# Kernel tuning notes

Hardware: AMD Instinct MI355X
Metric: run time of the kernel (lower is better)

Reference implementation:

```python
import jax, jax.numpy as jnp
import numpy as np

EPS = 1e-8
NU_MOLECULAR = 1.5e-05
# loss weights (module defaults)
DATA_W, BC_W, TURB_W, RANS_W, SMOOTH_W, WALL_W = 1.0, 0.05, 0.05, 0.05, 0.01, 0.02
CONT_INIT = CONT_TGT = 0.1
MOM_INIT = MOM_TGT = 0.1
RAMP_STEPS, RAMP_START = 1000, 0

N_NODES, N_EDGES = 100000, 6400000


def _curriculum_weights(step):
    if step < RAMP_START:
        return CONT_INIT, MOM_INIT
    if step >= RAMP_START + RAMP_STEPS:
        return CONT_TGT, MOM_TGT
    alpha = (step - RAMP_START) / RAMP_STEPS  # linear ramp
    return ((1 - alpha) * CONT_INIT + alpha * CONT_TGT,
            (1 - alpha) * MOM_INIT + alpha * MOM_TGT)


def setup_inputs() -> dict:
    key = jax.random.key(0)
    k1, k2, k3, k4, k5 = jax.random.split(key, 5)
    predictions = jax.random.normal(k1, (N_NODES, 4), dtype=jnp.float32)
    targets = jax.random.normal(k2, (N_NODES, 4), dtype=jnp.float32)
    # dx, dy strictly positive edge offsets
    edge_attr_dxdy = jax.random.uniform(k3, (N_EDGES, 2), dtype=jnp.float32, minval=1e-3, maxval=0.05)
    edge_index = jax.random.randint(k4, (2, N_EDGES), 0, N_NODES, dtype=jnp.int64)
    wall_mask = jax.random.bernoulli(k5, 0.05, (N_NODES,))
    return {"predictions": predictions, "targets": targets,
            "edge_attr_dxdy": edge_attr_dxdy, "edge_index": edge_index,
            "wall_mask": wall_mask, "step": 500}


def reference(predictions, targets, edge_attr_dxdy, edge_index, wall_mask, step):
    cont_w, mom_w = _curriculum_weights(int(step))
    N = predictions.shape[0]
    row, col = edge_index[0], edge_index[1]
    u, v, p, nu_t = (predictions[:, i] for i in range(4))
    dx, dy = edge_attr_dxdy[:, 0], edge_attr_dxdy[:, 1]

    # per-edge finite differences (single gather of node fields)
    du = u[col] - u[row]
    dv = v[col] - v[row]
    dp = p[col] - p[row]

    seg = lambda e: jax.ops.segment_sum(e, row, num_segments=N)
    edge_count = jnp.maximum(seg(jnp.ones_like(du)), 1.0)

    # --- data loss ---
    mse_loss = jnp.mean((predictions - targets) ** 2)

    # --- continuity (divergence) loss ---
    divergence = (seg(du / (dx + EPS)) + seg(dv / (dy + EPS))) / edge_count
    div_loss = jnp.mean(divergence ** 2)

    # --- momentum loss ---
    p_grad_x = seg(dp / (dx + EPS)) / edge_count
    p_grad_y = seg(dp / (dy + EPS)) / edge_count
    lap_u = seg(du / (dx ** 2 + EPS)) / edge_count
    lap_v = seg(dv / (dy ** 2 + EPS)) / edge_count
    nu_eff = NU_MOLECULAR + nu_t
    momentum_loss = jnp.mean((p_grad_x + nu_eff * lap_u) ** 2 +
                             (p_grad_y + nu_eff * lap_v) ** 2)

    # --- turbulence losses ---
    positivity_loss = jnp.mean(jax.nn.relu(-nu_t) ** 2)
    du_dx = du / (dx + EPS)
    du_dy = du / (dy + EPS)
    dv_dx = dv / (dx + EPS)
    dv_dy = dv / (dy + EPS)
    strain_sq_edge = 2.0 * (du_dx ** 2 + dv_dy ** 2) + (du_dy + dv_dx) ** 2
    strain_node = seg(strain_sq_edge) / edge_count
    production = nu_t * strain_node
    turb_production_loss = jnp.mean(production ** 2)
    turb_dissipation_loss = jnp.mean(nu_t ** 2)

    # --- boundary-condition & wall-function losses (wall mask) ---
    m = wall_mask.astype(u.dtype)
    n_wall = jnp.maximum(jnp.sum(m), 1.0)
    bc_loss = jnp.sum(m * (u ** 2 + v ** 2)) / n_wall
    wall_loss = jnp.sum(m * (u ** 2 + v ** 2 + nu_t ** 2)) / n_wall

    # --- smoothness loss over edges ---
    smooth_loss = jnp.mean((predictions[col] - predictions[row]) ** 2)

    total = (DATA_W * mse_loss + cont_w * div_loss + mom_w * momentum_loss +
             TURB_W * turb_production_loss + RANS_W * turb_dissipation_loss +
             BC_W * bc_loss + SMOOTH_W * smooth_loss + WALL_W * wall_loss)
    # positivity_loss is tracked but not weighted into total (per visible code paths)
    return total
```

## Files before the change

kernel.cpp:

```cpp
#include <hip/hip_runtime.h>
#include <hip/hip_fp16.h>

#define EPS 1e-8f
#define NU_MOL 1.5e-5f
#define NPB 512
#define MAXNB 256
#define NBP 256
#define NBLK 4096
#define CMAX 1664
#define KMAX 7
#define CH 2048
#define SPLIT 6
#define NGRP 64
#define GRP 64


union U32H2 { unsigned u; __half2 h; };

__device__ inline unsigned packh2(float a, float b) {
    U32H2 x; x.h = __halves2half2(__float2half_rn(a), __float2half_rn(b));
    return x.u;
}
__device__ inline float2 unpackh2(unsigned u) {
    U32H2 x; x.u = u;
    return make_float2(__low2float(x.h), __high2float(x.h));
}
__device__ inline unsigned bf16rne(float f) {
    unsigned u = __float_as_uint(f);
    u += 0x7FFFu + ((u >> 16) & 1u);
    return u >> 16;
}
__device__ inline float bf16dec(unsigned h) {
    return __uint_as_float(h << 16);
}


__global__ void detect_idx_dtype(const void* eidx, int N, int* flag) {
    const long long* ll = (const long long*)eidx;
    int is64 = 1;
    for (int i = 0; i < 16; ++i) {
        long long v = ll[i];
        if (v < 0 || v >= (long long)N) { is64 = 0; break; }
    }
    *flag = is64;
}

__global__ void finalize_kernel(const double* __restrict__ d,
                                const double* __restrict__ smooth_slots,
                                int N, int E, float* __restrict__ out)
{
    double smooth = 0.0;
    for (int i = 0; i < 64; ++i) smooth += smooth_slots[i];
    double dN = (double)N;
    double n_wall = d[5] > 1.0 ? d[5] : 1.0;
    double total = 1.0  * d[0] / (4.0 * dN)
                 + 0.1  * d[1] / dN
                 + 0.1  * d[2] / dN
                 + 0.05 * d[3] / dN
                 + 0.05 * d[4] / dN
                 + 0.05 * d[6] / n_wall
                 + 0.01 * smooth / (4.0 * (double)E)
                 + 0.02 * d[7] / n_wall;
    out[0] = (float)total;
}


__global__ __launch_bounds__(256) void count_kernel(
    const void* __restrict__ eidx, int E, int N, int NB,
    const int* __restrict__ flag, unsigned* __restrict__ counts)
{
    __shared__ unsigned hist[2][MAXNB];
    hist[0][threadIdx.x] = 0u;
    hist[1][threadIdx.x] = 0u;
    __syncthreads();
    const int w = (threadIdx.x >> 6) & 1;
    const int is64 = *flag;
    const long long* ll = (const long long*)eidx;
    const int* ii = (const int*)eidx;
    int chunk = (E + NBLK - 1) / NBLK;
    int s = blockIdx.x * chunk;
    int eend = min(E, s + chunk);
    for (int e = s + (int)threadIdx.x; e < eend; e += 256) {
        int r = is64 ? (int)ll[e] : ii[e];
        r = min(max(r, 0), N - 1);
        atomicAdd(&hist[w][r >> 9], 1u);
    }
    __syncthreads();
    if (threadIdx.x < NB)
        counts[(size_t)blockIdx.x * NBP + threadIdx.x] =
            hist[0][threadIdx.x] + hist[1][threadIdx.x];
}

__global__ __launch_bounds__(256) void group_sums_kernel(
    const unsigned* __restrict__ counts, unsigned* __restrict__ gsum, int NB)
{
    __shared__ unsigned red[4][64];
    int g = blockIdx.x;
    int b0 = blockIdx.y * 64;
    int j = threadIdx.x & 63, seg = threadIdx.x >> 6;
    int b = b0 + j;
    unsigned ssum = 0;
    if (b < NB) {
        #pragma unroll
        for (int k = 0; k < 16; ++k) {
            int row = g * GRP + seg * 16 + k;
            ssum += counts[(size_t)row * NBP + b];
        }
    }
    red[seg][j] = ssum;
    __syncthreads();
    if (seg == 0 && b < NB)
        gsum[(size_t)g * NBP + b] = red[0][j] + red[1][j] + red[2][j] + red[3][j];
}

__global__ __launch_bounds__(512) void scan_base_kernel(
    unsigned* __restrict__ gsum, unsigned* __restrict__ base, int NB)
{
    __shared__ unsigned sc[512];
    int t = threadIdx.x;
    unsigned total = 0;
    if (t < NB)
        for (int g = 0; g < NGRP; ++g) total += gsum[(size_t)g * NBP + t];
    sc[t] = total; __syncthreads();
    for (int off = 1; off < 512; off <<= 1) {
        unsigned x = (t >= off) ? sc[t - off] : 0u;
        __syncthreads();
        sc[t] += x;
        __syncthreads();
    }
    unsigned ex = sc[t] - total;
    if (t < NB) {
        base[t] = ex;
        unsigned run = ex;
        for (int g = 0; g < NGRP; ++g) {
            unsigned x = gsum[(size_t)g * NBP + t];
            gsum[(size_t)g * NBP + t] = run;
            run += x;
        }
    }
    if (t == 511) base[NB] = sc[511];
}

__global__ __launch_bounds__(256) void local_scan_kernel(
    unsigned* __restrict__ counts, const unsigned* __restrict__ gsum, int NB)
{
    __shared__ unsigned segs[4][64];
    int g = blockIdx.x;
    int b0 = blockIdx.y * 64;
    int j = threadIdx.x & 63, seg = threadIdx.x >> 6;
    int b = b0 + j;
    unsigned v[16];
    unsigned ssum = 0;
    if (b < NB) {
        #pragma unroll
        for (int k = 0; k < 16; ++k) {
            int row = g * GRP + seg * 16 + k;
            v[k] = counts[(size_t)row * NBP + b];
            ssum += v[k];
        }
    }
    segs[seg][j] = ssum;
    __syncthreads();
    if (b < NB) {
        unsigned carry = gsum[(size_t)g * NBP + b];
        for (int s_ = 0; s_ < seg; ++s_) carry += segs[s_][j];
        #pragma unroll
        for (int k = 0; k < 16; ++k) {
            int row = g * GRP + seg * 16 + k;
            counts[(size_t)row * NBP + b] = carry;
            carry += v[k];
        }
    }
}

__global__ __launch_bounds__(256) void scatter_kernel(
    const void* __restrict__ eidx, const float2* __restrict__ eattr,
    int E, int N, int NB, const int* __restrict__ flag,
    const unsigned* __restrict__ localoff ,
    uint2* __restrict__ vals)
{
    __shared__ unsigned hist[2][MAXNB];
    __shared__ unsigned cur[MAXNB];
    __shared__ unsigned gb2[MAXNB];
    __shared__ uint2 pl[CMAX];
    __shared__ unsigned char bb[CMAX];
    __shared__ unsigned wt[4];

    const int t = threadIdx.x;
    const int blk = blockIdx.x;
    const int lane = t & 63, wv = t >> 6;
    const int w = wv & 1;
    const int is64 = *flag;
    const long long* ll = (const long long*)eidx;
    const int* ii = (const int*)eidx;
    const int chunk = (E + NBLK - 1) / NBLK;
    const int s = blk * chunk;
    const int Cb = min(chunk, E - s);

    hist[0][t] = 0u;
    hist[1][t] = 0u;
    __syncthreads();

    unsigned rr[KMAX];
    #pragma unroll
    for (int k = 0; k < KMAX; ++k) {
        int i = k * 256 + t;
        if (i < Cb) {
            int r = is64 ? (int)ll[s + i] : ii[s + i];
            r = min(max(r, 0), N - 1);
            rr[k] = (unsigned)r;
            atomicAdd(&hist[w][r >> 9], 1u);
        } else rr[k] = 0xFFFFFFFFu;
    }
    if (t < NB) gb2[t] = localoff[(size_t)blk * NBP + t];
    __syncthreads();

    unsigned h = hist[0][t] + hist[1][t];
    unsigned x = h;
    #pragma unroll
    for (int off = 1; off < 64; off <<= 1) {
        unsigned y = (unsigned)__shfl_up((int)x, off, 64);
        if (lane >= off) x += y;
    }
    if (lane == 63) wt[wv] = x;
    __syncthreads();
    unsigned wadd = 0;
    for (int w2 = 0; w2 < wv; ++w2) wadd += wt[w2];
    unsigned ex = x + wadd - h;
    hist[0][t] = ex;
    cur[t] = ex;
    __syncthreads();
    if (t < NB) gb2[t] -= hist[0][t];
    __syncthreads();

    #pragma unroll
    for (int k = 0; k < KMAX; ++k) {
        int i = k * 256 + t;
        if (i >= Cb) break;
        int e = s + i;
        unsigned r = rr[k];
        unsigned b = r >> 9;
        unsigned rl = r & (NPB - 1);
        int c = is64 ? (int)ll[(long long)E + e] : ii[E + e];
        c = min(max(c, 0), N - 1);
        float2 dxy = eattr[e];
        unsigned pk = (unsigned)c | (rl << 17);
        unsigned pos = atomicAdd(&cur[b], 1u);
        pl[pos] = make_uint2(pk, packh2(dxy.x, dxy.y));
        bb[pos] = (unsigned char)b;
    }
    __syncthreads();

    #pragma unroll
    for (int k = 0; k < KMAX; ++k) {
        int p = k * 256 + t;
        if (p >= Cb) break;
        unsigned b = bb[p];
        vals[gb2[b] + (unsigned)p] = pl[p];
    }
}

__global__ __launch_bounds__(512) void accum_kernel(
    const uint2* __restrict__ vals, const unsigned* __restrict__ base,
    const float4* __restrict__ pred, int N,
    float* __restrict__ g , double* __restrict__ smooth_slots)
{
    __shared__ uint2 pl[CH];
    __shared__ uint2 ph[NPB];
    __shared__ unsigned hist[NPB];
    __shared__ unsigned cur[NPB];
    __shared__ unsigned wt[8];
    __shared__ double sm[8];

    const int b = blockIdx.x;
    const int t = threadIdx.x;
    const int wv = t >> 6, lane = t & 63;
    const int n0 = b * NPB;

    {
        int n = n0 + t;
        float4 p = (n < N) ? pred[n] : make_float4(0.f, 0.f, 0.f, 0.f);
        ph[t] = make_uint2(packh2(p.x, p.y), packh2(p.z, p.w));
    }

    unsigned s0 = base[b], e0 = base[b + 1];
    unsigned len = e0 - s0;
    unsigned s = s0 + (unsigned)(((unsigned long long)len * blockIdx.y) / SPLIT);
    unsigned e = s0 + (unsigned)(((unsigned long long)len * (blockIdx.y + 1)) / SPLIT);

    float cnt = 0, sdiv = 0, smx = 0, smy = 0, sstr = 0;
    double smooth = 0.0;

    for (unsigned cs = s; cs < e; cs += CH) {
        const int n = (int)min((unsigned)CH, e - cs);
        hist[t] = 0u;
        __syncthreads();

        uint2 vv[4];
        #pragma unroll
        for (int k = 0; k < 4; ++k) {
            int i = k * 512 + t;
            if (i < n) {
                vv[k] = vals[cs + i];
                atomicAdd(&hist[(vv[k].x >> 17) & (NPB - 1)], 1u);
            } else vv[k].x = 0xFFFFFFFFu;
        }
        __syncthreads();

        unsigned v = hist[t];
        unsigned x = v;
        #pragma unroll
        for (int off = 1; off < 64; off <<= 1) {
            unsigned y = (unsigned)__shfl_up((int)x, off, 64);
            if (lane >= off) x += y;
        }
        if (lane == 63) wt[wv] = x;
        __syncthreads();
        unsigned wadd = 0;
        for (int w = 0; w < wv; ++w) wadd += wt[w];
        unsigned incl = x + wadd;
        unsigned ex0 = incl - v;
        cur[t] = ex0;
        cnt += (float)v;
        __syncthreads();

        #pragma unroll
        for (int k = 0; k < 4; ++k) {
            int i = k * 512 + t;
            if (i >= n) break;
            unsigned pk = vv[k].x;
            int col = (int)(pk & 0x1FFFFu);
            unsigned rl = (pk >> 17) & (NPB - 1);
            float2 dxy = unpackh2(vv[k].y);
            float4 pc = pred[col];
            uint2 pru = ph[rl];
            float2 pxy = unpackh2(pru.x);
            float2 pzw = unpackh2(pru.y);
            float du = pc.x - pxy.x, dv = pc.y - pxy.y;
            float dp = pc.z - pzw.x, dn = pc.w - pzw.y;
            float rx  = 1.0f / (dxy.x + EPS);
            float ry  = 1.0f / (dxy.y + EPS);
            float rx2 = 1.0f / (dxy.x * dxy.x + EPS);
            float ry2 = 1.0f / (dxy.y * dxy.y + EPS);
            float du_dx = du * rx, du_dy = du * ry;
            float dv_dx = dv * rx, dv_dy = dv * ry;
            float nu_eff = NU_MOL + pzw.y;
            float sh = du_dy + dv_dx;
            float div_e = du_dx + dv_dy;
            float mx_e  = dp * rx + nu_eff * du * rx2;
            float my_e  = dp * ry + nu_eff * dv * ry2;
            float str_e = 2.0f * (du_dx * du_dx + dv_dy * dv_dy) + sh * sh;
            unsigned pos = atomicAdd(&cur[rl], 1u);
            pl[pos] = make_uint2(bf16rne(div_e) | (bf16rne(mx_e) << 16),
                                 bf16rne(my_e) | (bf16rne(str_e) << 16));
            smooth += (double)(du * du + dv * dv + dp * dp + dn * dn);
        }
        __syncthreads();

        for (unsigned i = ex0; i < incl; ++i) {
            uint2 pv = pl[i];
            sdiv += bf16dec(pv.x & 0xFFFFu);
            smx  += bf16dec(pv.x >> 16);
            smy  += bf16dec(pv.y & 0xFFFFu);
            sstr += bf16dec(pv.y >> 16);
        }
        __syncthreads();
    }

    {
        int n = n0 + t;
        if (n < N) {
            atomicAdd(&g[0 * (size_t)N + n], cnt);
            atomicAdd(&g[1 * (size_t)N + n], sdiv);
            atomicAdd(&g[2 * (size_t)N + n], smx);
            atomicAdd(&g[3 * (size_t)N + n], smy);
            atomicAdd(&g[4 * (size_t)N + n], sstr);
        }
    }

    for (int off = 32; off > 0; off >>= 1)
        smooth += __shfl_down(smooth, off);
    if (lane == 0) sm[wv] = smooth;
    __syncthreads();
    if (t == 0) {
        double tot = 0;
        #pragma unroll
        for (int w = 0; w < 8; ++w) tot += sm[w];
        atomicAdd(&smooth_slots[(b * SPLIT + blockIdx.y) & 63], tot);
    }
}

__global__ __launch_bounds__(256) void node_final_kernel(
    const float* __restrict__ g, const float4* __restrict__ pred,
    const float4* __restrict__ tgt, const unsigned char* __restrict__ wall,
    int N, double* __restrict__ d)
{
    int i = blockIdx.x * 256 + threadIdx.x;
    double v0 = 0, v1 = 0, v2 = 0, v3 = 0, v4 = 0, v5 = 0, v6 = 0, v7 = 0;
    if (i < N) {
        float cnt = g[0 * (size_t)N + i];
        float inv = 1.0f / fmaxf(cnt, 1.0f);
        float div = g[1 * (size_t)N + i] * inv;
        float mx  = g[2 * (size_t)N + i] * inv;
        float my  = g[3 * (size_t)N + i] * inv;
        float sn  = g[4 * (size_t)N + i] * inv;
        float4 p = pred[i];
        float4 tg = tgt[i];
        float prod = p.w * sn;
        float m = wall[i] ? 1.0f : 0.0f;
        float e0 = p.x - tg.x, e1 = p.y - tg.y, e2 = p.z - tg.z, e3 = p.w - tg.w;
        float uv = p.x * p.x + p.y * p.y;
        v0 = (double)(e0 * e0 + e1 * e1 + e2 * e2 + e3 * e3);
        v1 = (double)div * (double)div;
        v2 = (double)mx * (double)mx + (double)my * (double)my;
        v3 = (double)prod * (double)prod;
        v4 = (double)p.w * (double)p.w;
        v5 = (double)m;
        v6 = (double)(m * uv);
        v7 = (double)(m * (uv + p.w * p.w));
    }
    for (int off = 32; off > 0; off >>= 1) {
        v0 += __shfl_down(v0, off); v1 += __shfl_down(v1, off);
        v2 += __shfl_down(v2, off); v3 += __shfl_down(v3, off);
        v4 += __shfl_down(v4, off); v5 += __shfl_down(v5, off);
        v6 += __shfl_down(v6, off); v7 += __shfl_down(v7, off);
    }
    __shared__ double sm[4][8];
    int lane = threadIdx.x & 63, wv = threadIdx.x >> 6;
    if (lane == 0) {
        sm[wv][0] = v0; sm[wv][1] = v1; sm[wv][2] = v2; sm[wv][3] = v3;
        sm[wv][4] = v4; sm[wv][5] = v5; sm[wv][6] = v6; sm[wv][7] = v7;
    }
    __syncthreads();
    if (threadIdx.x < 8) {
        int q = threadIdx.x;
        atomicAdd(&d[q], sm[0][q] + sm[1][q] + sm[2][q] + sm[3][q]);
    }
}


__global__ __launch_bounds__(256) void edge_kernel(
    const void* __restrict__ eidx, const float2* __restrict__ eattr,
    const float4* __restrict__ pred, int E, int N, const int* __restrict__ flag,
    float* __restrict__ a_cnt, float* __restrict__ a_div,
    float* __restrict__ a_mx, float* __restrict__ a_my,
    float* __restrict__ a_str, double* __restrict__ smooth_slots)
{
    const int is64 = *flag;
    const long long* ll = (const long long*)eidx;
    const int* ii = (const int*)eidx;
    double smooth = 0.0;
    const int stride = gridDim.x * blockDim.x;
    for (int e = blockIdx.x * blockDim.x + threadIdx.x; e < E; e += stride) {
        int row, col;
        if (is64) { row = (int)ll[e]; col = (int)ll[(long long)E + e]; }
        else      { row = ii[e];      col = ii[E + e]; }
        row = min(max(row, 0), N - 1);
        col = min(max(col, 0), N - 1);
        float2 dxy = eattr[e];
        float4 pr = pred[row];
        float4 pc = pred[col];
        float du = pc.x - pr.x, dv = pc.y - pr.y;
        float dp = pc.z - pr.z, dn = pc.w - pr.w;
        float rx  = 1.0f / (dxy.x + EPS);
        float ry  = 1.0f / (dxy.y + EPS);
        float rx2 = 1.0f / (dxy.x * dxy.x + EPS);
        float ry2 = 1.0f / (dxy.y * dxy.y + EPS);
        float du_dx = du * rx, du_dy = du * ry;
        float dv_dx = dv * rx, dv_dy = dv * ry;
        float nu_eff = NU_MOL + pr.w;
        atomicAdd(&a_cnt[row], 1.0f);
        atomicAdd(&a_div[row], du_dx + dv_dy);
        atomicAdd(&a_mx[row], dp * rx + nu_eff * du * rx2);
        atomicAdd(&a_my[row], dp * ry + nu_eff * dv * ry2);
        float sh = du_dy + dv_dx;
        atomicAdd(&a_str[row], 2.0f * (du_dx * du_dx + dv_dy * dv_dy) + sh * sh);
        smooth += (double)(du * du + dv * dv + dp * dp + dn * dn);
    }
    for (int off = 32; off > 0; off >>= 1)
        smooth += __shfl_down(smooth, off);
    __shared__ double sm[4];
    int lane = threadIdx.x & 63, wv = threadIdx.x >> 6;
    if (lane == 0) sm[wv] = smooth;
    __syncthreads();
    if (threadIdx.x == 0)
        atomicAdd(&smooth_slots[blockIdx.x & 63], sm[0] + sm[1] + sm[2] + sm[3]);
}

__global__ __launch_bounds__(256) void node_kernel(
    const float4* __restrict__ pred, const float4* __restrict__ tgt,
    const unsigned char* __restrict__ wall, int N,
    const float* __restrict__ a_cnt, const float* __restrict__ a_div,
    const float* __restrict__ a_mx, const float* __restrict__ a_my,
    const float* __restrict__ a_str, double* __restrict__ d)
{
    int i = blockIdx.x * blockDim.x + threadIdx.x;
    double v0 = 0, v1 = 0, v2 = 0, v3 = 0, v4 = 0, v5 = 0, v6 = 0, v7 = 0;
    if (i < N) {
        float4 p = pred[i];
        float4 t = tgt[i];
        float inv = 1.0f / fmaxf(a_cnt[i], 1.0f);
        float div = a_div[i] * inv;
        float mx = a_mx[i] * inv, my = a_my[i] * inv;
        float sn = a_str[i] * inv;
        float prod = p.w * sn;
        float m = wall[i] ? 1.0f : 0.0f;
        float e0 = p.x - t.x, e1 = p.y - t.y, e2 = p.z - t.z, e3 = p.w - t.w;
        float uv = p.x * p.x + p.y * p.y;
        v0 = (double)(e0 * e0 + e1 * e1 + e2 * e2 + e3 * e3);
        v1 = (double)div * (double)div;
        v2 = (double)mx * (double)mx + (double)my * (double)my;
        v3 = (double)prod * (double)prod;
        v4 = (double)p.w * (double)p.w;
        v5 = (double)m;
        v6 = (double)(m * uv);
        v7 = (double)(m * (uv + p.w * p.w));
    }
    for (int off = 32; off > 0; off >>= 1) {
        v0 += __shfl_down(v0, off); v1 += __shfl_down(v1, off);
        v2 += __shfl_down(v2, off); v3 += __shfl_down(v3, off);
        v4 += __shfl_down(v4, off); v5 += __shfl_down(v5, off);
        v6 += __shfl_down(v6, off); v7 += __shfl_down(v7, off);
    }
    __shared__ double sm[4][8];
    int lane = threadIdx.x & 63, wv = threadIdx.x >> 6;
    if (lane == 0) {
        sm[wv][0] = v0; sm[wv][1] = v1; sm[wv][2] = v2; sm[wv][3] = v3;
        sm[wv][4] = v4; sm[wv][5] = v5; sm[wv][6] = v6; sm[wv][7] = v7;
    }
    __syncthreads();
    if (threadIdx.x < 8) {
        int q = threadIdx.x;
        atomicAdd(&d[q], sm[0][q] + sm[1][q] + sm[2][q] + sm[3][q]);
    }
}


extern "C" void kernel_launch(void* const* d_in, const int* in_sizes, int n_in,
                              void* d_out, int out_size, void* d_ws, size_t ws_size,
                              hipStream_t stream) {
    const float4* pred = (const float4*)d_in[0];
    const float4* tgt  = (const float4*)d_in[1];
    const float2* eattr = (const float2*)d_in[2];
    const void* eidx = d_in[3];
    const unsigned char* wall = (const unsigned char*)d_in[4];
    int N = in_sizes[0] / 4;
    int E = in_sizes[2] / 2;
    int NB = (N + NPB - 1) / NPB;
    int chunk = (E + NBLK - 1) / NBLK;
    int ntiles = (NB + 63) / 64;

    char* ws = (char*)d_ws;
    double* d = (double*)ws;
    double* smooth_slots = d + 8;
    int* flag = (int*)(ws + 576);

    size_t off = 1024;
    float* g        = (float*)(ws + off);     off += (size_t)5 * N * 4;
    unsigned* counts = (unsigned*)(ws + off); off += (size_t)NBLK * NBP * 4;
    unsigned* gsum   = (unsigned*)(ws + off); off += (size_t)NGRP * NBP * 4;
    unsigned* base   = (unsigned*)(ws + off); off += (size_t)(NB + 1) * 4;
    off = (off + 15) & ~(size_t)15;
    uint2* vals      = (uint2*)(ws + off);    off += (size_t)E * 8;
    size_t need_fast = off;

    bool fast = (NB <= MAXNB) && (N <= 131072) && (chunk <= CMAX) &&
                (ws_size >= need_fast);

    if (fast) {
        hipMemsetAsync(d_ws, 0, 1024 + (size_t)5 * N * 4, stream);
        detect_idx_dtype<<<1, 1, 0, stream>>>(eidx, N, flag);
        count_kernel<<<NBLK, 256, 0, stream>>>(eidx, E, N, NB, flag, counts);
        group_sums_kernel<<<dim3(NGRP, ntiles), 256, 0, stream>>>(counts, gsum, NB);
        scan_base_kernel<<<1, 512, 0, stream>>>(gsum, base, NB);
        local_scan_kernel<<<dim3(NGRP, ntiles), 256, 0, stream>>>(counts, gsum, NB);
        scatter_kernel<<<NBLK, 256, 0, stream>>>(eidx, eattr, E, N, NB, flag,
                                                 counts, vals);
        accum_kernel<<<dim3(NB, SPLIT), 512, 0, stream>>>(vals, base, pred, N,
                                                          g, smooth_slots);
        node_final_kernel<<<(N + 255) / 256, 256, 0, stream>>>(g, pred, tgt, wall,
                                                               N, d);
        finalize_kernel<<<1, 1, 0, stream>>>(d, smooth_slots, N, E, (float*)d_out);
    } else {
        float* arrays = (float*)(ws + 1024);
        float* a_cnt = arrays + (size_t)0 * N;
        float* a_div = arrays + (size_t)1 * N;
        float* a_mx  = arrays + (size_t)2 * N;
        float* a_my  = arrays + (size_t)3 * N;
        float* a_str = arrays + (size_t)4 * N;
        size_t zbytes = 1024 + (size_t)5 * N * sizeof(float);
        hipMemsetAsync(d_ws, 0, zbytes, stream);
        detect_idx_dtype<<<1, 1, 0, stream>>>(eidx, N, flag);
        edge_kernel<<<4096, 256, 0, stream>>>(eidx, eattr, pred, E, N, flag,
                                              a_cnt, a_div, a_mx, a_my, a_str,
                                              smooth_slots);
        node_kernel<<<(N + 255) / 256, 256, 0, stream>>>(pred, tgt, wall, N,
                                                         a_cnt, a_div, a_mx, a_my,
                                                         a_str, d);
        finalize_kernel<<<1, 1, 0, stream>>>(d, smooth_slots, N, E, (float*)d_out);
    }
}
```

Measured before the change: 239.8 us.

## Inline index dtype detection and batch loads ahead of atomics in scatter/accum

Drops the single-thread detect_idx_dtype launch, so each block now checks the first 16 indices itself. In count, scatter and accum, all global loads (row/col indices, edge attrs, vals, pred gathers) are issued before any LDS atomics, so memory latency can overlap. Slot positions come from the atomic return values instead of a second atomic pass. This removes one kernel launch and a barrier, but every block now re-reads 16 index values and uses more registers.

```diff
diff --git a/kernel.cpp b/kernel.cpp
--- a/kernel.cpp
+++ b/kernel.cpp
@@ -32,6 +32,17 @@
 }
 __device__ inline float bf16dec(unsigned h) {
     return __uint_as_float(h << 16);
+}
+
+__device__ inline int detect64(const void* eidx, int N) {
+    const long long* ll = (const long long*)eidx;
+    int is64 = 1;
+    #pragma unroll
+    for (int i = 0; i < 16; ++i) {
+        long long v = ll[i];
+        if (v < 0 || v >= (long long)N) is64 = 0;
+    }
+    return is64;
 }
 
 
@@ -67,24 +78,33 @@
 
 __global__ __launch_bounds__(256) void count_kernel(
     const void* __restrict__ eidx, int E, int N, int NB,
-    const int* __restrict__ flag, unsigned* __restrict__ counts)
+    unsigned* __restrict__ counts)
 {
     __shared__ unsigned hist[2][MAXNB];
     hist[0][threadIdx.x] = 0u;
     hist[1][threadIdx.x] = 0u;
     __syncthreads();
     const int w = (threadIdx.x >> 6) & 1;
-    const int is64 = *flag;
+    const int is64 = detect64(eidx, N);
     const long long* ll = (const long long*)eidx;
     const int* ii = (const int*)eidx;
     int chunk = (E + NBLK - 1) / NBLK;
     int s = blockIdx.x * chunk;
-    int eend = min(E, s + chunk);
-    for (int e = s + (int)threadIdx.x; e < eend; e += 256) {
-        int r = is64 ? (int)ll[e] : ii[e];
-        r = min(max(r, 0), N - 1);
-        atomicAdd(&hist[w][r >> 9], 1u);
-    }
+    int Cb = min(chunk, E - s);
+
+    unsigned rr[KMAX];
+    #pragma unroll
+    for (int k = 0; k < KMAX; ++k) {
+        int i = k * 256 + threadIdx.x;
+        if (i < Cb) {
+            int r = is64 ? (int)ll[s + i] : ii[s + i];
+            rr[k] = (unsigned)min(max(r, 0), N - 1);
+        } else rr[k] = 0xFFFFFFFFu;
+    }
+    #pragma unroll
+    for (int k = 0; k < KMAX; ++k)
+        if (rr[k] != 0xFFFFFFFFu)
+            atomicAdd(&hist[w][rr[k] >> 9], 1u);
     __syncthreads();
     if (threadIdx.x < NB)
         counts[(size_t)blockIdx.x * NBP + threadIdx.x] =
@@ -118,9 +138,15 @@
 {
     __shared__ unsigned sc[512];
     int t = threadIdx.x;
+    unsigned vg[NGRP];
     unsigned total = 0;
-    if (t < NB)
-        for (int g = 0; g < NGRP; ++g) total += gsum[(size_t)g * NBP + t];
+    if (t < NB) {
+        #pragma unroll
+        for (int g = 0; g < NGRP; ++g) {
+            vg[g] = gsum[(size_t)g * NBP + t];
+            total += vg[g];
+        }
+    }
     sc[t] = total; __syncthreads();
     for (int off = 1; off < 512; off <<= 1) {
         unsigned x = (t >= off) ? sc[t - off] : 0u;
@@ -132,8 +158,9 @@
     if (t < NB) {
         base[t] = ex;
         unsigned run = ex;
+        #pragma unroll
         for (int g = 0; g < NGRP; ++g) {
-            unsigned x = gsum[(size_t)g * NBP + t];
+            unsigned x = vg[g];
             gsum[(size_t)g * NBP + t] = run;
             run += x;
         }
@@ -175,7 +202,7 @@
 
 __global__ __launch_bounds__(256) void scatter_kernel(
     const void* __restrict__ eidx, const float2* __restrict__ eattr,
-    int E, int N, int NB, const int* __restrict__ flag,
+    int E, int N, int NB,
     const unsigned* __restrict__ localoff ,
     uint2* __restrict__ vals)
 {
@@ -190,7 +217,7 @@
     const int blk = blockIdx.x;
     const int lane = t & 63, wv = t >> 6;
     const int w = wv & 1;
-    const int is64 = *flag;
+    const int is64 = detect64(eidx, N);
     const long long* ll = (const long long*)eidx;
     const int* ii = (const int*)eidx;
     const int chunk = (E + NBLK - 1) / NBLK;
@@ -201,17 +228,19 @@
     hist[1][t] = 0u;
     __syncthreads();
 
-    unsigned rr[KMAX];
+    unsigned rr[KMAX], rk[KMAX];
     #pragma unroll
     for (int k = 0; k < KMAX; ++k) {
         int i = k * 256 + t;
         if (i < Cb) {
             int r = is64 ? (int)ll[s + i] : ii[s + i];
-            r = min(max(r, 0), N - 1);
-            rr[k] = (unsigned)r;
-            atomicAdd(&hist[w][r >> 9], 1u);
+            rr[k] = (unsigned)min(max(r, 0), N - 1);
         } else rr[k] = 0xFFFFFFFFu;
     }
+    #pragma unroll
+    for (int k = 0; k < KMAX; ++k)
+        if (rr[k] != 0xFFFFFFFFu)
+            rk[k] = atomicAdd(&hist[w][rr[k] >> 9], 1u);
     if (t < NB) gb2[t] = localoff[(size_t)blk * NBP + t];
     __syncthreads();
 
@@ -227,36 +256,46 @@
     unsigned wadd = 0;
     for (int w2 = 0; w2 < wv; ++w2) wadd += wt[w2];
     unsigned ex = x + wadd - h;
-    hist[0][t] = ex;
     cur[t] = ex;
     __syncthreads();
-    if (t < NB) gb2[t] -= hist[0][t];
-    __syncthreads();
-
+    if (t < NB) gb2[t] -= cur[t];
+
+    int cc[KMAX]; float2 dd[KMAX];
     #pragma unroll
     for (int k = 0; k < KMAX; ++k) {
         int i = k * 256 + t;
-        if (i >= Cb) break;
-        int e = s + i;
-        unsigned r = rr[k];
-        unsigned b = r >> 9;
-        unsigned rl = r & (NPB - 1);
-        int c = is64 ? (int)ll[(long long)E + e] : ii[E + e];
-        c = min(max(c, 0), N - 1);
-        float2 dxy = eattr[e];
-        unsigned pk = (unsigned)c | (rl << 17);
-        unsigned pos = atomicAdd(&cur[b], 1u);
-        pl[pos] = make_uint2(pk, packh2(dxy.x, dxy.y));
-        bb[pos] = (unsigned char)b;
-    }
-    __syncthreads();
-
+        if (i < Cb) {
+            int e = s + i;
+            cc[k] = is64 ? (int)ll[(long long)E + e] : ii[E + e];
+            dd[k] = eattr[e];
+        }
+    }
+    #pragma unroll
+    for (int k = 0; k < KMAX; ++k) {
+        int i = k * 256 + t;
+        if (i < Cb) {
+            unsigned r = rr[k];
+            unsigned b = r >> 9;
+            unsigned rl = r & (NPB - 1);
+            int c = min(max(cc[k], 0), N - 1);
+            unsigned slot = cur[b] + (w ? hist[0][b] : 0u) + rk[k];
+            pl[slot] = make_uint2((unsigned)c | (rl << 17),
+                                  packh2(dd[k].x, dd[k].y));
+            bb[slot] = (unsigned char)b;
+        }
+    }
+    __syncthreads();
+
+    uint2 op[KMAX]; unsigned ob[KMAX];
     #pragma unroll
     for (int k = 0; k < KMAX; ++k) {
         int p = k * 256 + t;
-        if (p >= Cb) break;
-        unsigned b = bb[p];
-        vals[gb2[b] + (unsigned)p] = pl[p];
+        if (p < Cb) { op[k] = pl[p]; ob[k] = (unsigned)bb[p]; }
+    }
+    #pragma unroll
+    for (int k = 0; k < KMAX; ++k) {
+        int p = k * 256 + t;
+        if (p < Cb) vals[gb2[ob[k]] + (unsigned)p] = op[k];
     }
 }
 
@@ -296,14 +335,20 @@
         hist[t] = 0u;
         __syncthreads();
 
-        uint2 vv[4];
+        uint2 vv[4]; unsigned rk2[4]; float4 pcc[4];
+        #pragma unroll
+        for (int k = 0; k < 4; ++k) {
+            int i = k * 512 + t;
+            if (i < n) vv[k] = vals[cs + i];
+            else vv[k].x = 0xFFFFFFFFu;
+        }
         #pragma unroll
         for (int k = 0; k < 4; ++k) {
             int i = k * 512 + t;
             if (i < n) {
-                vv[k] = vals[cs + i];
-                atomicAdd(&hist[(vv[k].x >> 17) & (NPB - 1)], 1u);
-            } else vv[k].x = 0xFFFFFFFFu;
+                rk2[k] = atomicAdd(&hist[(vv[k].x >> 17) & (NPB - 1)], 1u);
+                pcc[k] = pred[vv[k].x & 0x1FFFFu];
+            }
         }
         __syncthreads();
 
@@ -327,12 +372,11 @@
         #pragma unroll
         for (int k = 0; k < 4; ++k) {
             int i = k * 512 + t;
-            if (i >= n) break;
+            if (i >= n) continue;
             unsigned pk = vv[k].x;
-            int col = (int)(pk & 0x1FFFFu);
             unsigned rl = (pk >> 17) & (NPB - 1);
             float2 dxy = unpackh2(vv[k].y);
-            float4 pc = pred[col];
+            float4 pc = pcc[k];
             uint2 pru = ph[rl];
             float2 pxy = unpackh2(pru.x);
             float2 pzw = unpackh2(pru.y);
@@ -350,7 +394,7 @@
             float mx_e  = dp * rx + nu_eff * du * rx2;
             float my_e  = dp * ry + nu_eff * dv * ry2;
             float str_e = 2.0f * (du_dx * du_dx + dv_dy * dv_dy) + sh * sh;
-            unsigned pos = atomicAdd(&cur[rl], 1u);
+            unsigned pos = cur[rl] + rk2[k];
             pl[pos] = make_uint2(bf16rne(div_e) | (bf16rne(mx_e) << 16),
                                  bf16rne(my_e) | (bf16rne(str_e) << 16));
             smooth += (double)(du * du + dv * dv + dp * dp + dn * dn);
@@ -569,12 +613,11 @@
 
     if (fast) {
         hipMemsetAsync(d_ws, 0, 1024 + (size_t)5 * N * 4, stream);
-        detect_idx_dtype<<<1, 1, 0, stream>>>(eidx, N, flag);
-        count_kernel<<<NBLK, 256, 0, stream>>>(eidx, E, N, NB, flag, counts);
+        count_kernel<<<NBLK, 256, 0, stream>>>(eidx, E, N, NB, counts);
         group_sums_kernel<<<dim3(NGRP, ntiles), 256, 0, stream>>>(counts, gsum, NB);
         scan_base_kernel<<<1, 512, 0, stream>>>(gsum, base, NB);
         local_scan_kernel<<<dim3(NGRP, ntiles), 256, 0, stream>>>(counts, gsum, NB);
-        scatter_kernel<<<NBLK, 256, 0, stream>>>(eidx, eattr, E, N, NB, flag,
+        scatter_kernel<<<NBLK, 256, 0, stream>>>(eidx, eattr, E, N, NB,
                                                  counts, vals);
         accum_kernel<<<dim3(NB, SPLIT), 512, 0, stream>>>(vals, base, pred, N,
                                                           g, smooth_slots);
```

After: 236.7 us. No clear change (-1.3%).
